# Kernel tuning notes

Measured on AMD Instinct MI355X. Metric: run time of the kernel, lower is better.

The kernel has to match this reference:

```python
import jax, jax.numpy as jnp
import numpy as np

H, C = 8, 32          # heads, per-head channels
N, E = 100000, 1600000
NEG_SLOPE = 0.2
LN_EPS = 1e-5


def layer_norm(x, g, b):
    mu = jnp.mean(x, axis=-1, keepdims=True)
    var = jnp.mean((x - mu) ** 2, axis=-1, keepdims=True)
    return (x - mu) * jax.lax.rsqrt(var + LN_EPS) * g + b


def setup_inputs() -> dict:
    key = jax.random.key(0)
    ks = jax.random.split(key, 8)
    x = jax.random.normal(ks[0], (N, C), dtype=jnp.float32)
    edge_index = jax.random.randint(ks[1], (2, E), 0, N, dtype=jnp.int64)
    s = 1.0 / np.sqrt(C)
    W_gat = jax.random.normal(ks[2], (C, H * C), dtype=jnp.float32) * s
    att_src = jax.random.normal(ks[3], (H, C), dtype=jnp.float32) * s
    att_dst = jax.random.normal(ks[4], (H, C), dtype=jnp.float32) * s
    bias_gat = jnp.zeros((C,), jnp.float32)
    w1 = jax.random.normal(ks[5], (C, 128), dtype=jnp.float32) * s
    b1 = jnp.zeros((128,), jnp.float32)
    w2 = jax.random.normal(ks[6], (128, C), dtype=jnp.float32) / np.sqrt(128)
    b2 = jnp.zeros((C,), jnp.float32)
    g1 = jnp.ones((C,), jnp.float32); be1 = jnp.zeros((C,), jnp.float32)
    g2 = jnp.ones((C,), jnp.float32); be2 = jnp.zeros((C,), jnp.float32)
    return dict(x=x, edge_index=edge_index, W_gat=W_gat, att_src=att_src,
                att_dst=att_dst, bias_gat=bias_gat, w1=w1, b1=b1, w2=w2,
                b2=b2, g1=g1, be1=be1, g2=g2, be2=be2)


def gat_conv(x, edge_index, W_gat, att_src, att_dst, bias_gat):
    n = x.shape[0]
    # add self loops (PyG default)
    loops = jnp.arange(n, dtype=edge_index.dtype)
    ei = jnp.concatenate([edge_index, jnp.stack([loops, loops])], axis=1)
    src, dst = ei[0], ei[1]
    xp = (x @ W_gat).reshape(n, H, C)                      # [N,H,C]
    a_src = jnp.einsum('nhc,hc->nh', xp, att_src)          # [N,H]
    a_dst = jnp.einsum('nhc,hc->nh', xp, att_dst)
    alpha = jax.nn.leaky_relu(a_src[src] + a_dst[dst], NEG_SLOPE)  # [E',H]
    # segment softmax over incoming edges of each dst node
    m = jax.ops.segment_max(alpha, dst, num_segments=n)
    ea = jnp.exp(alpha - m[dst])
    denom = jax.ops.segment_sum(ea, dst, num_segments=n)
    attn = ea / (denom[dst] + 1e-16)                       # [E',H]
    msg = xp[src] * attn[..., None]                        # [E',H,C]
    out = jax.ops.segment_sum(msg, dst, num_segments=n)    # [N,H,C]
    return out.mean(axis=1) + bias_gat                     # concat=False -> head mean


def reference(x, edge_index, W_gat, att_src, att_dst, bias_gat,
              w1, b1, w2, b2, g1, be1, g2, be2):
    h = gat_conv(x, edge_index, W_gat, att_src, att_dst, bias_gat)
    h = layer_norm(h + x, g1, be1)
    ff = jax.nn.relu(h @ w1 + b1) @ w2 + b2
    return layer_norm(ff + h, g2, be2)
```

## Files before the change

### kernel.cpp

```cpp
#include <hip/hip_runtime.h>
#include <hip/hip_fp16.h>
#include <stdint.h>

#define HH 8
#define CC 32
#define HC 256
#define FF 128
#define NEG 0.2f
#define LNEPS 1e-5f

typedef __attribute__((ext_vector_type(8))) short bf16x8;
typedef __attribute__((ext_vector_type(4))) float f32x4;
typedef unsigned short u16;

__device__ inline unsigned bf16r(float f) {
  unsigned u = __float_as_uint(f);
  return (u + 0x7fffu + ((u >> 16) & 1u)) >> 16;
}
__device__ inline float bflo(unsigned w) { return __uint_as_float(w << 16); }
__device__ inline float bfhi(unsigned w) { return __uint_as_float(w & 0xffff0000u); }
__device__ inline float leaky(float v) { return v >= 0.f ? v : NEG * v; }
__device__ inline float h2f(unsigned hbits) {
  return __half2float(__ushort_as_half((unsigned short)hbits));
}
__device__ inline u16 f2h(float f) {
  return __half_as_ushort(__float2half(f));
}
__device__ inline float ub0(unsigned w) { return (float)(w & 0xffu); }
__device__ inline float ub1(unsigned w) { return (float)((w >> 8) & 0xffu); }
__device__ inline float ub2(unsigned w) { return (float)((w >> 16) & 0xffu); }
__device__ inline float ub3(unsigned w) { return (float)(w >> 24); }

__global__ __launch_bounds__(256) void klayout(
    const float* __restrict__ W, const float* __restrict__ atts,
    const float* __restrict__ attd, const float* __restrict__ w1,
    const float* __restrict__ w2,
    u16* __restrict__ Wb, u16* __restrict__ Zb,
    u16* __restrict__ V1b, u16* __restrict__ V2b, u16* __restrict__ WSb)
{
  int t = threadIdx.x;
  for (int i = t; i < 16 * 512; i += 256) {
    int j = i & 7, l = (i >> 3) & 63, nb = i >> 9;
    int k = 8 * (l >> 4) + j, c = 16 * nb + (l & 15);
    Wb[i] = (u16)bf16r(W[k * HC + c]);
  }
  for (int i = t; i < 8 * 512; i += 256) {
    int j = i & 7, l = (i >> 3) & 63, kb = i >> 9;
    int k = 32 * kb + 8 * (l >> 4) + j;
    int tc = l & 15;
    float v = 0.f;
    if (tc < 8)  { if ((k >> 5) == tc)     v = atts[tc * 32 + (k & 31)]; }
    else         { if ((k >> 5) == tc - 8) v = attd[(tc - 8) * 32 + (k & 31)]; }
    Zb[i] = (u16)bf16r(v);
  }
  for (int i = t; i < 8 * 512; i += 256) {
    int j = i & 7, l = (i >> 3) & 63, nb = i >> 9;
    int k = 8 * (l >> 4) + j, c = 16 * nb + (l & 15);
    V1b[i] = (u16)bf16r(w1[k * FF + c]);
  }
  for (int i = t; i < 8 * 512; i += 256) {
    int j = i & 7, l = (i >> 3) & 63, kn = i >> 9;
    int kb = kn >> 1, nb2 = kn & 1;
    int k = 32 * kb + 8 * (l >> 4) + j, c = 16 * nb2 + (l & 15);
    V2b[i] = (u16)bf16r(w2[k * CC + c]);
  }
  for (int i = t; i < 16 * 512; i += 256) {
    int j = i & 7, l = (i >> 3) & 63, kn = i >> 9;
    int kb = kn >> 1, nb2 = kn & 1;
    int krow = kb * 32 + 8 * (l >> 4) + j;
    int h = krow >> 5, kk = krow & 31;
    int c = 16 * nb2 + (l & 15);
    WSb[i] = (u16)bf16r(W[kk * HC + h * 32 + c]);
  }
}

__global__ __launch_bounds__(256) void khist(
    const int* __restrict__ ei, int e, int n,
    int* __restrict__ deg4, unsigned* __restrict__ dstr)
{
  int r = (int)blockIdx.x & 3;
  int* dr = deg4 + (size_t)r * n;
  int i = (int)blockIdx.x * 1024 + (int)threadIdx.x * 4;
  if (i >= e) return;
  const int* dst = ei + e;
  if (i + 3 < e) {
    int4 d4 = *(const int4*)(dst + i);
    unsigned r0 = (unsigned)atomicAdd(&dr[d4.x], 1);
    unsigned r1 = (unsigned)atomicAdd(&dr[d4.y], 1);
    unsigned r2 = (unsigned)atomicAdd(&dr[d4.z], 1);
    unsigned r3 = (unsigned)atomicAdd(&dr[d4.w], 1);
    uint4 o;
    o.x = (unsigned)d4.x | ((unsigned)r << 17) | (r0 << 19);
    o.y = (unsigned)d4.y | ((unsigned)r << 17) | (r1 << 19);
    o.z = (unsigned)d4.z | ((unsigned)r << 17) | (r2 << 19);
    o.w = (unsigned)d4.w | ((unsigned)r << 17) | (r3 << 19);
    *(uint4*)(dstr + i) = o;
  } else {
    for (int k = 0; k < 4 && i + k < e; ++k) {
      int d = dst[i + k];
      unsigned rr = (unsigned)atomicAdd(&dr[d], 1);
      dstr[i + k] = (unsigned)d | ((unsigned)r << 17) | (rr << 19);
    }
  }
}

__global__ __launch_bounds__(256) void k1c(
    const float* __restrict__ x, const u16* __restrict__ Wb,
    const u16* __restrict__ Zb,
    unsigned* __restrict__ xqx, unsigned* __restrict__ ascp,
    float* __restrict__ a_d, int n)
{
  __shared__ u16 lt[4][16 * 264];
  int wid = threadIdx.x >> 6, lane = threadIdx.x & 63;
  int q = lane & 15, g = lane >> 4;
  long node0 = (long)((int)blockIdx.x * 4 + wid) * 16;
  if (node0 + 16 > n) node0 = n - 16;
  u16* L = lt[wid];
  u16* ascp16 = (u16*)ascp;

  const float* xr = x + (node0 + q) * CC + 8 * g;
  float4 xa = *(const float4*)xr, xb = *(const float4*)(xr + 4);
  bf16x8 af;
  af[0] = (short)bf16r(xa.x); af[1] = (short)bf16r(xa.y);
  af[2] = (short)bf16r(xa.z); af[3] = (short)bf16r(xa.w);
  af[4] = (short)bf16r(xb.x); af[5] = (short)bf16r(xb.y);
  af[6] = (short)bf16r(xb.z); af[7] = (short)bf16r(xb.w);

  float mx = fmaxf(fmaxf(fmaxf(fabsf(xa.x), fabsf(xa.y)), fmaxf(fabsf(xa.z), fabsf(xa.w))),
                   fmaxf(fmaxf(fabsf(xb.x), fabsf(xb.y)), fmaxf(fabsf(xb.z), fabsf(xb.w))));
  mx = fmaxf(mx, __shfl_xor(mx, 16));
  mx = fmaxf(mx, __shfl_xor(mx, 32));
  float rinv = (mx > 0.f) ? 127.f / mx : 0.f;
  u16 sch = f2h(mx * (1.f / 127.f));
  ascp16[((node0 + q) * HH + 2 * g) * 2 + 1]     = sch;
  ascp16[((node0 + q) * HH + 2 * g + 1) * 2 + 1] = sch;
  {
    int q0 = min(max(__float2int_rn(xa.x * rinv), -127), 127) + 128;
    int q1 = min(max(__float2int_rn(xa.y * rinv), -127), 127) + 128;
    int q2 = min(max(__float2int_rn(xa.z * rinv), -127), 127) + 128;
    int q3 = min(max(__float2int_rn(xa.w * rinv), -127), 127) + 128;
    int q4 = min(max(__float2int_rn(xb.x * rinv), -127), 127) + 128;
    int q5 = min(max(__float2int_rn(xb.y * rinv), -127), 127) + 128;
    int q6 = min(max(__float2int_rn(xb.z * rinv), -127), 127) + 128;
    int q7 = min(max(__float2int_rn(xb.w * rinv), -127), 127) + 128;
    uint2 pk;
    pk.x = (unsigned)q0 | ((unsigned)q1 << 8) | ((unsigned)q2 << 16) | ((unsigned)q3 << 24);
    pk.y = (unsigned)q4 | ((unsigned)q5 << 8) | ((unsigned)q6 << 16) | ((unsigned)q7 << 24);
    *(uint2*)(xqx + (node0 + q) * 8 + 2 * g) = pk;
  }

#pragma unroll
  for (int nb = 0; nb < 16; ++nb) {
    bf16x8 bf = *(const bf16x8*)(Wb + nb * 512 + lane * 8);
    f32x4 acc = {0.f, 0.f, 0.f, 0.f};
    acc = __builtin_amdgcn_mfma_f32_16x16x32_bf16(af, bf, acc, 0, 0, 0);
    int col = 16 * nb + q;
#pragma unroll
    for (int r = 0; r < 4; ++r)
      L[(4 * g + r) * 264 + col] = (u16)bf16r(acc[r]);
  }
  __syncthreads();

  f32x4 az = {0.f, 0.f, 0.f, 0.f};
#pragma unroll
  for (int kb = 0; kb < 8; ++kb) {
    bf16x8 a2 = *(const bf16x8*)(L + q * 264 + kb * 32 + g * 8);
    bf16x8 zb = *(const bf16x8*)(Zb + kb * 512 + lane * 8);
    az = __builtin_amdgcn_mfma_f32_16x16x32_bf16(a2, zb, az, 0, 0, 0);
  }
  int hq = q & 7;
  if (q < 8) {
#pragma unroll
    for (int r = 0; r < 4; ++r)
      ascp16[((node0 + 4 * g + r) * HH + hq) * 2] = (u16)bf16r(az[r]);
  } else {
#pragma unroll
    for (int r = 0; r < 4; ++r)
      a_d[(node0 + 4 * g + r) * HH + hq] = az[r];
  }
}

__global__ __launch_bounds__(256) void kscanA(const int* __restrict__ deg4,
                                              int* __restrict__ bsum, int n)
{
  __shared__ int ws[4];
  int t = threadIdx.x;
  int i = (int)blockIdx.x * 1024 + t * 4;
  int s = 0;
  if (i + 3 < n) {
#pragma unroll
    for (int r = 0; r < 4; ++r) {
      int4 v = *(const int4*)(deg4 + (size_t)r * n + i);
      s += v.x + v.y + v.z + v.w;
    }
  } else {
    for (int k = 0; k < 4 && i + k < n; ++k)
#pragma unroll
      for (int r = 0; r < 4; ++r) s += deg4[(size_t)r * n + i + k];
  }
#pragma unroll
  for (int mask = 1; mask < 64; mask <<= 1) s += __shfl_xor(s, mask);
  if ((t & 63) == 0) ws[t >> 6] = s;
  __syncthreads();
  if (t == 0) bsum[blockIdx.x] = ws[0] + ws[1] + ws[2] + ws[3];
}

__global__ __launch_bounds__(1024) void kscanB(int* __restrict__ bsum, int nb)
{
  __shared__ int wsum[16];
  int t = threadIdx.x, lane = t & 63, wid = t >> 6;
  int v = (t < nb) ? bsum[t] : 0;
  int s = v;
#pragma unroll
  for (int d = 1; d < 64; d <<= 1) { int tt = __shfl_up(s, d); if (lane >= d) s += tt; }
  if (lane == 63) wsum[wid] = s;
  __syncthreads();
  if (wid == 0) {
    int w = (lane < 16) ? wsum[lane] : 0;
#pragma unroll
    for (int d = 1; d < 16; d <<= 1) { int tt = __shfl_up(w, d); if (lane >= d) w += tt; }
    if (lane < 16) wsum[lane] = w;
  }
  __syncthreads();
  int excl = s - v + ((wid > 0) ? wsum[wid - 1] : 0);
  if (t < nb) bsum[t] = excl;
}

__global__ __launch_bounds__(256) void kscanC(const int* __restrict__ deg4,
                                              const int* __restrict__ bsum,
                                              int* __restrict__ rb,
                                              int* __restrict__ degt, int n)
{
  __shared__ int ws[4];
  int t = threadIdx.x, lane = t & 63, wid = t >> 6;
  int i = (int)blockIdx.x * 1024 + t * 4;
  int c0[4] = {0,0,0,0}, c1[4] = {0,0,0,0}, c2[4] = {0,0,0,0}, c3[4] = {0,0,0,0};
  if (i + 3 < n) {
    int4 v0 = *(const int4*)(deg4 + 0 * (size_t)n + i);
    int4 v1 = *(const int4*)(deg4 + 1 * (size_t)n + i);
    int4 v2 = *(const int4*)(deg4 + 2 * (size_t)n + i);
    int4 v3 = *(const int4*)(deg4 + 3 * (size_t)n + i);
    c0[0]=v0.x;c0[1]=v0.y;c0[2]=v0.z;c0[3]=v0.w;
    c1[0]=v1.x;c1[1]=v1.y;c1[2]=v1.z;c1[3]=v1.w;
    c2[0]=v2.x;c2[1]=v2.y;c2[2]=v2.z;c2[3]=v2.w;
    c3[0]=v3.x;c3[1]=v3.y;c3[2]=v3.z;c3[3]=v3.w;
  } else {
    for (int k = 0; k < 4 && i + k < n; ++k) {
      c0[k] = deg4[0 * (size_t)n + i + k];
      c1[k] = deg4[1 * (size_t)n + i + k];
      c2[k] = deg4[2 * (size_t)n + i + k];
      c3[k] = deg4[3 * (size_t)n + i + k];
    }
  }
  int tot[4];
#pragma unroll
  for (int k = 0; k < 4; ++k) tot[k] = c0[k] + c1[k] + c2[k] + c3[k];
  int tsum = tot[0] + tot[1] + tot[2] + tot[3];
  int s = tsum;
#pragma unroll
  for (int d = 1; d < 64; d <<= 1) { int tt = __shfl_up(s, d); if (lane >= d) s += tt; }
  if (lane == 63) ws[wid] = s;
  __syncthreads();
  if (t == 0) {
    int a = ws[0]; ws[0] = 0;
    int b = ws[1]; ws[1] = a; a += b;
    int c = ws[2]; ws[2] = a; a += c;
    ws[3] = a;
  }
  __syncthreads();
  int base = bsum[blockIdx.x] + ws[wid] + (s - tsum);
#pragma unroll
  for (int k = 0; k < 4; ++k) {
    if (i + k < n) {
      int b0 = base;
      rb[0 * (size_t)n + i + k] = b0;
      rb[1 * (size_t)n + i + k] = b0 + c0[k];
      rb[2 * (size_t)n + i + k] = b0 + c0[k] + c1[k];
      rb[3 * (size_t)n + i + k] = b0 + c0[k] + c1[k] + c2[k];
      degt[i + k] = tot[k];
    }
    base += tot[k];
  }
}

__global__ __launch_bounds__(256) void kscatter(
    const int* __restrict__ ei, const unsigned* __restrict__ dstr, int e,
    const int* __restrict__ rb, int* __restrict__ csr, int n)
{
  int oct = (int)blockIdx.x & 3;
  int nsub = (int)gridDim.x >> 2;
  int sub = (int)blockIdx.x >> 2;
  int nper = (n + 3) >> 2;
  int lo = oct * nper, hi = lo + nper;
  int stride = nsub << 10;
  for (int i = (sub * 256 + (int)threadIdx.x) * 4; i < e; i += stride) {
    if (i + 3 < e) {
      uint4 d4 = *(const uint4*)(dstr + i);
      int4 s4 = *(const int4*)(ei + i);
      int dx = d4.x & 0x1ffff, dy = d4.y & 0x1ffff,
          dz = d4.z & 0x1ffff, dw = d4.w & 0x1ffff;
      if (dx >= lo && dx < hi)
        csr[rb[(size_t)((d4.x >> 17) & 3) * n + dx] + (d4.x >> 19)] = s4.x;
      if (dy >= lo && dy < hi)
        csr[rb[(size_t)((d4.y >> 17) & 3) * n + dy] + (d4.y >> 19)] = s4.y;
      if (dz >= lo && dz < hi)
        csr[rb[(size_t)((d4.z >> 17) & 3) * n + dz] + (d4.z >> 19)] = s4.z;
      if (dw >= lo && dw < hi)
        csr[rb[(size_t)((d4.w >> 17) & 3) * n + dw] + (d4.w >> 19)] = s4.w;
    } else {
      for (int k = 0; k < 4 && i + k < e; ++k) {
        unsigned dv = dstr[i + k];
        int d = dv & 0x1ffff;
        if (d >= lo && d < hi)
          csr[rb[(size_t)((dv >> 17) & 3) * n + d] + (dv >> 19)] = ei[i + k];
      }
    }
  }
}

__global__ __launch_bounds__(256) void kagg(
    const int* __restrict__ csr, const int* __restrict__ offs,
    const int* __restrict__ degt,
    const unsigned* __restrict__ ascp, const float* __restrict__ a_d,
    const unsigned* __restrict__ xqx, unsigned* __restrict__ agg32, int n)
{
  int lane = threadIdx.x & 63;
  int wid  = threadIdx.x >> 6;
  int base = ((int)blockIdx.x * 4 + wid) * 4;
  int eg = lane >> 3, ha = lane & 7;
  int hb = eg;
  int c4 = lane & 7;

  for (int t = 0; t < 4; ++t) {
    int node = base + t;
    if (node >= n) return;
    int start = offs[node];
    int dg = degt[node];
    unsigned aw_self = ascp[(size_t)node * HH + ha];
    float ad_a  = a_d[(size_t)node * HH + ha];
    float aself = leaky(bflo(aw_self) + ad_a);

    float acc0 = 0.f, acc1 = 0.f, acc2 = 0.f, acc3 = 0.f;
    float dnA = 0.f, osA = 0.f;

    for (int j0 = 0; j0 < dg; j0 += 8) {
      int cnt = dg - j0; if (cnt > 8) cnt = 8;
      int idx = j0 + eg;
      int srcl = 0; float pw = 0.f;
      if (idx < dg) {
        srcl = csr[start + idx];
        unsigned av = ascp[(size_t)srcl * HH + ha];
        float al = leaky(bflo(av) + ad_a);
        float p  = __expf(al - aself);
        pw = p * h2f(av >> 16);
        dnA += p; osA += pw;
      }
      if (cnt == 8) {
#pragma unroll
        for (int j = 0; j < 8; ++j) {
          float wt = __shfl(pw, (j << 3) + hb);
          int s = __shfl(srcl, j << 3);
          unsigned w = xqx[(size_t)s * 8 + c4];
          acc0 = fmaf(ub0(w), wt, acc0);
          acc1 = fmaf(ub1(w), wt, acc1);
          acc2 = fmaf(ub2(w), wt, acc2);
          acc3 = fmaf(ub3(w), wt, acc3);
        }
      } else {
        for (int j = 0; j < cnt; ++j) {
          float wt = __shfl(pw, (j << 3) + hb);
          int s = __shfl(srcl, j << 3);
          unsigned w = xqx[(size_t)s * 8 + c4];
          acc0 = fmaf(ub0(w), wt, acc0);
          acc1 = fmaf(ub1(w), wt, acc1);
          acc2 = fmaf(ub2(w), wt, acc2);
          acc3 = fmaf(ub3(w), wt, acc3);
        }
      }
    }

    float dnH = dnA, osH = osA;
    dnH += __shfl_xor(dnH, 8);  osH += __shfl_xor(osH, 8);
    dnH += __shfl_xor(dnH, 16); osH += __shfl_xor(osH, 16);
    dnH += __shfl_xor(dnH, 32); osH += __shfl_xor(osH, 32);
    float dnB = __shfl(dnH, hb);
    float osB = __shfl(osH, hb);
    float scB = __shfl(h2f(aw_self >> 16), hb);

    {
      unsigned w = xqx[(size_t)node * 8 + c4];
      dnB += 1.f; osB += scB;
      acc0 = fmaf(ub0(w), scB, acc0);
      acc1 = fmaf(ub1(w), scB, acc1);
      acc2 = fmaf(ub2(w), scB, acc2);
      acc3 = fmaf(ub3(w), scB, acc3);
    }

    float corr = -128.f * osB;
    float inv = 0.125f / dnB;
    acc0 = (acc0 + corr) * inv;
    acc1 = (acc1 + corr) * inv;
    acc2 = (acc2 + corr) * inv;
    acc3 = (acc3 + corr) * inv;
    uint2 pk;
    pk.x = bf16r(acc0) | (bf16r(acc1) << 16);
    pk.y = bf16r(acc2) | (bf16r(acc3) << 16);
    *(uint2*)(agg32 + (size_t)node * 128 + hb * 16 + c4 * 2) = pk;
  }
}

__global__ __launch_bounds__(256) void k5m(
    const u16* __restrict__ agg16, const float* __restrict__ x,
    const float* __restrict__ bg, const u16* __restrict__ WSb,
    const u16* __restrict__ V1b, const u16* __restrict__ V2b,
    const float* __restrict__ b1, const float* __restrict__ b2,
    const float* __restrict__ g1, const float* __restrict__ be1,
    const float* __restrict__ g2, const float* __restrict__ be2,
    float* __restrict__ out, int n)
{
  __shared__ u16   lh[4][16 * 40];
  __shared__ u16   lf[4][16 * 136];
  __shared__ float lo[4][16 * 36];
  int wid = threadIdx.x >> 6, lane = threadIdx.x & 63;
  int q = lane & 15, g = lane >> 4;
  long node0 = (long)((int)blockIdx.x * 4 + wid) * 16;
  if (node0 + 16 > n) node0 = n - 16;
  u16* LH = lh[wid]; u16* LF = lf[wid]; float* LO = lo[wid];

  {
    int row = lane >> 2, off = (lane & 3) * 8;
    const float* x8 = x + (node0 + row) * CC + off;
    float4 c0 = *(const float4*)x8, c1 = *(const float4*)(x8 + 4);
    float4 bg0 = *(const float4*)(bg + off), bg1 = *(const float4*)(bg + off + 4);
    float4 s0 = make_float4(c0.x + bg0.x, c0.y + bg0.y, c0.z + bg0.z, c0.w + bg0.w);
    float4 s1 = make_float4(c1.x + bg1.x, c1.y + bg1.y, c1.z + bg1.z, c1.w + bg1.w);
    *(float4*)(LO + row * 36 + off)     = s0;
    *(float4*)(LO + row * 36 + off + 4) = s1;
  }
  __syncthreads();

  {
    f32x4 a20 = {0.f, 0.f, 0.f, 0.f}, a21 = {0.f, 0.f, 0.f, 0.f};
#pragma unroll
    for (int kb = 0; kb < 8; ++kb) {
      bf16x8 af = *(const bf16x8*)(agg16 + (node0 + q) * 256 + kb * 32 + g * 8);
      bf16x8 w0 = *(const bf16x8*)(WSb + (kb * 2 + 0) * 512 + lane * 8);
      bf16x8 w1v = *(const bf16x8*)(WSb + (kb * 2 + 1) * 512 + lane * 8);
      a20 = __builtin_amdgcn_mfma_f32_16x16x32_bf16(af, w0, a20, 0, 0, 0);
      a21 = __builtin_amdgcn_mfma_f32_16x16x32_bf16(af, w1v, a21, 0, 0, 0);
    }
#pragma unroll
    for (int r = 0; r < 4; ++r) {
      LO[(4 * g + r) * 36 + q]      += a20[r];
      LO[(4 * g + r) * 36 + 16 + q] += a21[r];
    }
  }
  __syncthreads();

  float hv[32];
  if (lane < 16) {
#pragma unroll
    for (int i = 0; i < 8; ++i) {
      float4 t = *(const float4*)(LO + q * 36 + i * 4);
      hv[4*i] = t.x; hv[4*i+1] = t.y; hv[4*i+2] = t.z; hv[4*i+3] = t.w;
    }
    float mu = 0.f;
#pragma unroll
    for (int c = 0; c < 32; ++c) mu += hv[c];
    mu *= (1.f / 32.f);
    float var = 0.f;
#pragma unroll
    for (int c = 0; c < 32; ++c) { float t = hv[c] - mu; var = fmaf(t, t, var); }
    float rs = rsqrtf(var * (1.f / 32.f) + LNEPS);
#pragma unroll
    for (int c = 0; c < 32; ++c) hv[c] = (hv[c] - mu) * rs * g1[c] + be1[c];
    uint* dst = (uint*)(LH + q * 40);
#pragma unroll
    for (int i = 0; i < 16; ++i)
      dst[i] = bf16r(hv[2*i]) | (bf16r(hv[2*i+1]) << 16);
  }
  __syncthreads();

  bf16x8 ah = *(const bf16x8*)(LH + q * 40 + g * 8);
#pragma unroll
  for (int nb = 0; nb < 8; ++nb) {
    bf16x8 v1 = *(const bf16x8*)(V1b + nb * 512 + lane * 8);
    f32x4 acc = {0.f, 0.f, 0.f, 0.f};
    acc = __builtin_amdgcn_mfma_f32_16x16x32_bf16(ah, v1, acc, 0, 0, 0);
    int col = 16 * nb + q;
    float bias = b1[col];
#pragma unroll
    for (int r = 0; r < 4; ++r) {
      float f = fmaxf(acc[r] + bias, 0.f);
      LF[(4 * g + r) * 136 + col] = (u16)bf16r(f);
    }
  }
  __syncthreads();

  f32x4 a20 = {0.f, 0.f, 0.f, 0.f}, a21 = {0.f, 0.f, 0.f, 0.f};
#pragma unroll
  for (int kb = 0; kb < 4; ++kb) {
    bf16x8 af2 = *(const bf16x8*)(LF + q * 136 + kb * 32 + g * 8);
    bf16x8 v20 = *(const bf16x8*)(V2b + (kb * 2 + 0) * 512 + lane * 8);
    bf16x8 v21 = *(const bf16x8*)(V2b + (kb * 2 + 1) * 512 + lane * 8);
    a20 = __builtin_amdgcn_mfma_f32_16x16x32_bf16(af2, v20, a20, 0, 0, 0);
    a21 = __builtin_amdgcn_mfma_f32_16x16x32_bf16(af2, v21, a21, 0, 0, 0);
  }
  __syncthreads();
#pragma unroll
  for (int r = 0; r < 4; ++r) {
    LO[(4 * g + r) * 36 + q]      = a20[r];
    LO[(4 * g + r) * 36 + 16 + q] = a21[r];
  }
  __syncthreads();

  if (lane < 16) {
    float ov[32];
#pragma unroll
    for (int i = 0; i < 8; ++i) {
      float4 t = *(const float4*)(LO + q * 36 + i * 4);
      ov[4*i] = t.x; ov[4*i+1] = t.y; ov[4*i+2] = t.z; ov[4*i+3] = t.w;
    }
#pragma unroll
    for (int c = 0; c < 32; ++c) ov[c] += b2[c] + hv[c];
    float mu2 = 0.f;
#pragma unroll
    for (int c = 0; c < 32; ++c) mu2 += ov[c];
    mu2 *= (1.f / 32.f);
    float var2 = 0.f;
#pragma unroll
    for (int c = 0; c < 32; ++c) { float t = ov[c] - mu2; var2 = fmaf(t, t, var2); }
    float rs2 = rsqrtf(var2 * (1.f / 32.f) + LNEPS);
    float* op = out + (node0 + q) * CC;
#pragma unroll
    for (int i = 0; i < 8; ++i) {
      float4 o;
      o.x = (ov[4*i]   - mu2) * rs2 * g2[4*i]   + be2[4*i];
      o.y = (ov[4*i+1] - mu2) * rs2 * g2[4*i+1] + be2[4*i+1];
      o.z = (ov[4*i+2] - mu2) * rs2 * g2[4*i+2] + be2[4*i+2];
      o.w = (ov[4*i+3] - mu2) * rs2 * g2[4*i+3] + be2[4*i+3];
      *(float4*)(op + i * 4) = o;
    }
  }
}

extern "C" void kernel_launch(void* const* d_in, const int* in_sizes, int n_in,
                              void* d_out, int out_size, void* d_ws, size_t ws_size,
                              hipStream_t stream)
{
  const float* x    = (const float*)d_in[0];
  const int*   ei   = (const int*)d_in[1];
  const float* W    = (const float*)d_in[2];
  const float* atts = (const float*)d_in[3];
  const float* attd = (const float*)d_in[4];
  const float* bg   = (const float*)d_in[5];
  const float* w1   = (const float*)d_in[6];
  const float* b1   = (const float*)d_in[7];
  const float* w2   = (const float*)d_in[8];
  const float* b2   = (const float*)d_in[9];
  const float* g1   = (const float*)d_in[10];
  const float* be1  = (const float*)d_in[11];
  const float* g2   = (const float*)d_in[12];
  const float* be2  = (const float*)d_in[13];

  int n = in_sizes[0] / CC;
  int e = in_sizes[1] / 2;

  uint8_t* ws = (uint8_t*)d_ws;
  size_t o = 0;
  unsigned* xqx = (unsigned*)(ws + o); o += (size_t)n * 32;
  unsigned* ascp = (unsigned*)(ws + o); o += (size_t)n * HH * 4;
  float* a_d = (float*)(ws + o); o += (size_t)n * HH * 4;
  unsigned* agg32 = (unsigned*)(ws + o); o += (size_t)n * 512;
  int* deg4   = (int*)(ws + o); o += (size_t)n * 4 * 4;
  int* rb     = (int*)(ws + o); o += (size_t)n * 4 * 4;
  int* degt   = (int*)(ws + o); o += (size_t)n * 4;
  unsigned* dstr = (unsigned*)(ws + o); o += (size_t)e * 4;
  int* csr    = (int*)(ws + o); o += (size_t)e * 4;
  int* bsum   = (int*)(ws + o); o += 4096;
  u16* Wb  = (u16*)(ws + o); o += 16 * 512 * 2;
  u16* Zb  = (u16*)(ws + o); o += 8 * 512 * 2;
  u16* V1b = (u16*)(ws + o); o += 8 * 512 * 2;
  u16* V2b = (u16*)(ws + o); o += 8 * 512 * 2;
  u16* WSb = (u16*)(ws + o); o += 16 * 512 * 2;

  (void)hipMemsetAsync(deg4, 0, (size_t)n * 4 * 4, stream);

  int nwaves = (n + 15) / 16;
  int nbc   = (nwaves + 3) / 4;
  int nb_e4 = (e + 1023) / 1024;
  int nb_s  = (n + 1023) / 1024;
  int nb_ag = (n + 15) / 16;

  khist   <<<nb_e4, 256, 0, stream>>>(ei, e, n, deg4, dstr);
  klayout <<<1, 256, 0, stream>>>(W, atts, attd, w1, w2, Wb, Zb, V1b, V2b, WSb);
  k1c     <<<nbc, 256, 0, stream>>>(x, Wb, Zb, xqx, ascp, a_d, n);
  kscanA  <<<nb_s, 256, 0, stream>>>(deg4, bsum, n);
  kscanB  <<<1, 1024, 0, stream>>>(bsum, nb_s);
  kscanC  <<<nb_s, 256, 0, stream>>>(deg4, bsum, rb, degt, n);
  kscatter<<<512, 256, 0, stream>>>(ei, dstr, e, rb, csr, n);
  kagg    <<<nb_ag, 256, 0, stream>>>(csr, rb, degt, ascp, a_d, xqx, agg32, n);
  k5m     <<<nbc, 256, 0, stream>>>((const u16*)agg32, x, bg, WSb, V1b, V2b,
                                    b1, b2, g1, be1, g2, be2, (float*)d_out, n);
}
```

Before: 246.0 us.

## Fuse degree histogram into node projection kernel and parallelize weight layout

The edge-destination histogram kernel is merged into the node projection kernel as extra blocks, so both independent workloads run in one launch and overlap on the GPU. The weight layout kernel now uses 16 blocks with a grid-stride loop instead of a single block. The aggregation loop also broadcasts each source index from the per-head lane rather than lane j*8, which gives each lane its own shuffle source. Mixing atomic-heavy blocks with MFMA blocks in one kernel may change occupancy, since the histogram blocks now reserve the projection kernel's shared memory.

Measured after the change: 231.1 us. -6.0%, faster.

```diff
diff --git a/kernel.cpp b/kernel.cpp
--- a/kernel.cpp
+++ b/kernel.cpp
@@ -38,13 +38,14 @@
     u16* __restrict__ Wb, u16* __restrict__ Zb,
     u16* __restrict__ V1b, u16* __restrict__ V2b, u16* __restrict__ WSb)
 {
-  int t = threadIdx.x;
-  for (int i = t; i < 16 * 512; i += 256) {
+  int t0 = (int)blockIdx.x * 256 + (int)threadIdx.x;
+  int st = (int)gridDim.x * 256;
+  for (int i = t0; i < 16 * 512; i += st) {
     int j = i & 7, l = (i >> 3) & 63, nb = i >> 9;
     int k = 8 * (l >> 4) + j, c = 16 * nb + (l & 15);
     Wb[i] = (u16)bf16r(W[k * HC + c]);
   }
-  for (int i = t; i < 8 * 512; i += 256) {
+  for (int i = t0; i < 8 * 512; i += st) {
     int j = i & 7, l = (i >> 3) & 63, kb = i >> 9;
     int k = 32 * kb + 8 * (l >> 4) + j;
     int tc = l & 15;
@@ -53,18 +54,18 @@
     else         { if ((k >> 5) == tc - 8) v = attd[(tc - 8) * 32 + (k & 31)]; }
     Zb[i] = (u16)bf16r(v);
   }
-  for (int i = t; i < 8 * 512; i += 256) {
+  for (int i = t0; i < 8 * 512; i += st) {
     int j = i & 7, l = (i >> 3) & 63, nb = i >> 9;
     int k = 8 * (l >> 4) + j, c = 16 * nb + (l & 15);
     V1b[i] = (u16)bf16r(w1[k * FF + c]);
   }
-  for (int i = t; i < 8 * 512; i += 256) {
+  for (int i = t0; i < 8 * 512; i += st) {
     int j = i & 7, l = (i >> 3) & 63, kn = i >> 9;
     int kb = kn >> 1, nb2 = kn & 1;
     int k = 32 * kb + 8 * (l >> 4) + j, c = 16 * nb2 + (l & 15);
     V2b[i] = (u16)bf16r(w2[k * CC + c]);
   }
-  for (int i = t; i < 16 * 512; i += 256) {
+  for (int i = t0; i < 16 * 512; i += st) {
     int j = i & 7, l = (i >> 3) & 63, kn = i >> 9;
     int kb = kn >> 1, nb2 = kn & 1;
     int krow = kb * 32 + 8 * (l >> 4) + j;
@@ -74,42 +75,41 @@
   }
 }
 
-__global__ __launch_bounds__(256) void khist(
-    const int* __restrict__ ei, int e, int n,
-    int* __restrict__ deg4, unsigned* __restrict__ dstr)
-{
-  int r = (int)blockIdx.x & 3;
-  int* dr = deg4 + (size_t)r * n;
-  int i = (int)blockIdx.x * 1024 + (int)threadIdx.x * 4;
-  if (i >= e) return;
-  const int* dst = ei + e;
-  if (i + 3 < e) {
-    int4 d4 = *(const int4*)(dst + i);
-    unsigned r0 = (unsigned)atomicAdd(&dr[d4.x], 1);
-    unsigned r1 = (unsigned)atomicAdd(&dr[d4.y], 1);
-    unsigned r2 = (unsigned)atomicAdd(&dr[d4.z], 1);
-    unsigned r3 = (unsigned)atomicAdd(&dr[d4.w], 1);
-    uint4 o;
-    o.x = (unsigned)d4.x | ((unsigned)r << 17) | (r0 << 19);
-    o.y = (unsigned)d4.y | ((unsigned)r << 17) | (r1 << 19);
-    o.z = (unsigned)d4.z | ((unsigned)r << 17) | (r2 << 19);
-    o.w = (unsigned)d4.w | ((unsigned)r << 17) | (r3 << 19);
-    *(uint4*)(dstr + i) = o;
-  } else {
-    for (int k = 0; k < 4 && i + k < e; ++k) {
-      int d = dst[i + k];
-      unsigned rr = (unsigned)atomicAdd(&dr[d], 1);
-      dstr[i + k] = (unsigned)d | ((unsigned)r << 17) | (rr << 19);
-    }
-  }
-}
-
 __global__ __launch_bounds__(256) void k1c(
     const float* __restrict__ x, const u16* __restrict__ Wb,
-    const u16* __restrict__ Zb,
+    const u16* __restrict__ Zb, const int* __restrict__ ei,
     unsigned* __restrict__ xqx, unsigned* __restrict__ ascp,
-    float* __restrict__ a_d, int n)
-{
+    float* __restrict__ a_d, int* __restrict__ deg4,
+    unsigned* __restrict__ dstr, int n, int e, int nbc)
+{
+  if ((int)blockIdx.x >= nbc) {
+    int bi = (int)blockIdx.x - nbc;
+    int r = bi & 3;
+    int* dr = deg4 + (size_t)r * n;
+    int i = bi * 1024 + (int)threadIdx.x * 4;
+    if (i >= e) return;
+    const int* dst = ei + e;
+    if (i + 3 < e) {
+      int4 d4 = *(const int4*)(dst + i);
+      unsigned r0 = (unsigned)atomicAdd(&dr[d4.x], 1);
+      unsigned r1 = (unsigned)atomicAdd(&dr[d4.y], 1);
+      unsigned r2 = (unsigned)atomicAdd(&dr[d4.z], 1);
+      unsigned r3 = (unsigned)atomicAdd(&dr[d4.w], 1);
+      uint4 o;
+      o.x = (unsigned)d4.x | ((unsigned)r << 17) | (r0 << 19);
+      o.y = (unsigned)d4.y | ((unsigned)r << 17) | (r1 << 19);
+      o.z = (unsigned)d4.z | ((unsigned)r << 17) | (r2 << 19);
+      o.w = (unsigned)d4.w | ((unsigned)r << 17) | (r3 << 19);
+      *(uint4*)(dstr + i) = o;
+    } else {
+      for (int k = 0; k < 4 && i + k < e; ++k) {
+        int d = dst[i + k];
+        unsigned rr = (unsigned)atomicAdd(&dr[d], 1);
+        dstr[i + k] = (unsigned)d | ((unsigned)r << 17) | (rr << 19);
+      }
+    }
+    return;
+  }
   __shared__ u16 lt[4][16 * 264];
   int wid = threadIdx.x >> 6, lane = threadIdx.x & 63;
   int q = lane & 15, g = lane >> 4;
@@ -358,8 +358,9 @@
       if (cnt == 8) {
 #pragma unroll
         for (int j = 0; j < 8; ++j) {
-          float wt = __shfl(pw, (j << 3) + hb);
-          int s = __shfl(srcl, j << 3);
+          int sl = (j << 3) + hb;
+          float wt = __shfl(pw, sl);
+          int s = __shfl(srcl, sl);
           unsigned w = xqx[(size_t)s * 8 + c4];
           acc0 = fmaf(ub0(w), wt, acc0);
           acc1 = fmaf(ub1(w), wt, acc1);
@@ -368,8 +369,9 @@
         }
       } else {
         for (int j = 0; j < cnt; ++j) {
-          float wt = __shfl(pw, (j << 3) + hb);
-          int s = __shfl(srcl, j << 3);
+          int sl = (j << 3) + hb;
+          float wt = __shfl(pw, sl);
+          int s = __shfl(srcl, sl);
           unsigned w = xqx[(size_t)s * 8 + c4];
           acc0 = fmaf(ub0(w), wt, acc0);
           acc1 = fmaf(ub1(w), wt, acc1);
@@ -592,9 +594,9 @@
   int nb_s  = (n + 1023) / 1024;
   int nb_ag = (n + 15) / 16;
 
-  khist   <<<nb_e4, 256, 0, stream>>>(ei, e, n, deg4, dstr);
-  klayout <<<1, 256, 0, stream>>>(W, atts, attd, w1, w2, Wb, Zb, V1b, V2b, WSb);
-  k1c     <<<nbc, 256, 0, stream>>>(x, Wb, Zb, xqx, ascp, a_d, n);
+  klayout <<<16, 256, 0, stream>>>(W, atts, attd, w1, w2, Wb, Zb, V1b, V2b, WSb);
+  k1c     <<<nbc + nb_e4, 256, 0, stream>>>(x, Wb, Zb, ei, xqx, ascp, a_d, deg4,
+                                            dstr, n, e, nbc);
   kscanA  <<<nb_s, 256, 0, stream>>>(deg4, bsum, n);
   kscanB  <<<1, 1024, 0, stream>>>(bsum, nb_s);
   kscanC  <<<nb_s, 256, 0, stream>>>(deg4, bsum, rb, degt, n);
```
